# Kernel optimization log

Measured on AMD Instinct MI355X. Metric: run time of the kernel, lower is better.

The kernel has to match this reference:

```python
import jax, jax.numpy as jnp
import numpy as np

B_SZ, L, D_MODEL = 2, 2048, 2048
INTER, HEADS, P, N, G, K = 4096, 64, 64, 128, 1, 4
CONV_DIM = INTER + 2 * G * N
EPS = 1e-5


def silu(x):
    return x * jax.nn.sigmoid(x)


def softplus_thresh(x, threshold=10.0):
    # matches source: where(x < thr, log(1+exp(x)), x)
    return jnp.where(x < threshold, jnp.log1p(jnp.exp(jnp.minimum(x, threshold))), x)


def setup_inputs() -> dict:
    key = jax.random.key(0)
    ks = jax.random.split(key, 8)
    s = 0.02
    return {
        "hidden_states": jax.random.normal(ks[0], (B_SZ, L, D_MODEL), jnp.float32),
        "W_z": jax.random.normal(ks[1], (D_MODEL, INTER), jnp.float32) * s,
        "W_xBC": jax.random.normal(ks[2], (D_MODEL, CONV_DIM), jnp.float32) * s,
        "W_dt": jax.random.normal(ks[3], (D_MODEL, HEADS), jnp.float32) * s,
        "conv_w": jax.random.normal(ks[4], (CONV_DIM, K), jnp.float32) * 0.1,
        "conv_b": jnp.zeros((CONV_DIM,), jnp.float32),
        "dt_bias": jax.random.uniform(ks[5], (HEADS,), jnp.float32, -2.0, 0.0),
        "A_log": jnp.log(jnp.arange(1, HEADS + 1, dtype=jnp.float32)),
        "D": jnp.ones((HEADS,), jnp.float32),
        "norm_w": jnp.ones((INTER,), jnp.float32),
        "W_out": jax.random.normal(ks[6], (INTER, D_MODEL), jnp.float32) * s,
    }


def reference(hidden_states, W_z, W_xBC, W_dt, conv_w, conv_b, dt_bias, A_log, D, norm_w, W_out):
    b, l, _ = hidden_states.shape
    Hg = HEADS // G  # heads per group

    gate = hidden_states @ W_z                      # [b,l,INTER]
    xBC = hidden_states @ W_xBC                     # [b,l,CONV_DIM]
    dt = softplus_thresh(hidden_states @ W_dt + dt_bias)  # [b,l,H]

    # causal depthwise conv1d + silu (padding=K-1, truncated to seq_len)
    xp = jnp.pad(xBC, ((0, 0), (K - 1, 0), (0, 0)))
    kern = jnp.transpose(conv_w)[:, None, :]        # [K,1,CONV_DIM] (WIO)
    xBC = jax.lax.conv_general_dilated(
        xp, kern, (1,), 'VALID',
        dimension_numbers=('NWC', 'WIO', 'NWC'),
        feature_group_count=CONV_DIM)
    xBC = silu(xBC + conv_b)

    gns = G * N
    x = xBC[..., :INTER].reshape(b, l, G, Hg, P)
    Bm = xBC[..., INTER:INTER + gns].reshape(b, l, G, N)
    Cm = xBC[..., INTER + gns:].reshape(b, l, G, N)

    A = -jnp.exp(A_log)                             # [H]
    dA = jnp.exp(dt * A).reshape(b, l, G, Hg)       # [b,l,G,Hg]
    dtx = dt.reshape(b, l, G, Hg)[..., None] * x    # [b,l,G,Hg,P]

    def step(state, inp):
        dA_t, dtx_t, B_t, C_t = inp
        # state: [b,G,Hg,P,N]
        state = state * dA_t[..., None, None] + dtx_t[..., None] * B_t[:, :, None, None, :]
        y_t = jnp.einsum('bghpn,bgn->bghp', state, C_t)
        return state, y_t

    xs = (jnp.moveaxis(dA, 1, 0), jnp.moveaxis(dtx, 1, 0),
          jnp.moveaxis(Bm, 1, 0), jnp.moveaxis(Cm, 1, 0))
    state0 = jnp.zeros((b, G, Hg, P, N), jnp.float32)
    _, ys = jax.lax.scan(step, state0, xs)          # [l,b,G,Hg,P]
    y = jnp.moveaxis(ys, 0, 1) + D.reshape(G, Hg)[..., None] * x
    scan_out = y.reshape(b, l, INTER)

    # gated RMSNorm within groups
    hs = scan_out.reshape(b, l, G, INTER // G).astype(jnp.float32)
    gt = gate.reshape(b, l, G, INTER // G).astype(jnp.float32)
    hs = hs * silu(gt)
    var = jnp.mean(hs * hs, axis=-1, keepdims=True)
    hs = hs * jax.lax.rsqrt(var + EPS)
    normed = norm_w * hs.reshape(b, l, INTER)

    return normed @ W_out
```

## Files before the change

kernel.cpp:

```cpp
#include <hip/hip_runtime.h>
#include <hip/hip_bf16.h>
#include <math.h>

typedef unsigned short u16;
typedef unsigned int   u32;
typedef __attribute__((ext_vector_type(8))) short short8;
typedef __attribute__((ext_vector_type(4))) float f32x4;

#define B_SZ     2
#define LSEQ     2048
#define DMODEL   2048
#define INTER    4096
#define HEADS    64
#define NSTATE   128
#define CONV_DIM 4352
#define XSTR     8576
#define NFUSE    8576
#define EPS      1e-5f
#define QCH      64
#define NCHUNK   (LSEQ / QCH)

__device__ __forceinline__ float bf2f(u16 u) {
    u32 v = ((u32)u) << 16;
    return __builtin_bit_cast(float, v);
}
__device__ __forceinline__ u16 f2bf(float x) {
    __hip_bfloat16 h = __float2bfloat16(x);
    return __builtin_bit_cast(u16, h);
}
__device__ __forceinline__ u32 pack2(float lo, float hi) {
    return (u32)f2bf(lo) | ((u32)f2bf(hi) << 16);
}
__device__ __forceinline__ void gl2lds16(const void* g, void* l) {
    __builtin_amdgcn_global_load_lds(
        (const __attribute__((address_space(1))) u32*)g,
        (__attribute__((address_space(3))) u32*)l, 16, 0, 0);
}

__global__ __launch_bounds__(256) void cvt_f32_bf16(
    const float* __restrict__ in, u16* __restrict__ out, int n4)
{
    int i = blockIdx.x * 256 + threadIdx.x;
    if (i >= n4) return;
    float4 v = ((const float4*)in)[i];
    ushort4 o;
    o.x = f2bf(v.x); o.y = f2bf(v.y); o.z = f2bf(v.z); o.w = f2bf(v.w);
    ((ushort4*)out)[i] = o;
}

__global__ __launch_bounds__(256) void tr_f32_bf16(
    const float* __restrict__ in, u16* __restrict__ out, int R, int C)
{
    __shared__ u16 tile[64][68];
    const int r0 = blockIdx.y * 64, c0 = blockIdx.x * 64;
    const int tr = threadIdx.x >> 4, tc = (threadIdx.x & 15) * 4;
    #pragma unroll
    for (int i = 0; i < 4; ++i) {
        int r = tr + i * 16;
        float4 v = *(const float4*)(in + (size_t)(r0 + r) * C + c0 + tc);
        tile[r][tc + 0] = f2bf(v.x);
        tile[r][tc + 1] = f2bf(v.y);
        tile[r][tc + 2] = f2bf(v.z);
        tile[r][tc + 3] = f2bf(v.w);
    }
    __syncthreads();
    #pragma unroll
    for (int i = 0; i < 4; ++i) {
        int oc = tr + i * 16;
        ushort4 o;
        o.x = tile[tc + 0][oc];
        o.y = tile[tc + 1][oc];
        o.z = tile[tc + 2][oc];
        o.w = tile[tc + 3][oc];
        *(ushort4*)(out + (size_t)(c0 + oc) * R + r0 + tc) = o;
    }
}

template<int OUT_BF16>
__global__ __launch_bounds__(256) void gemm_nt(
    const u16* __restrict__ A, const u16* __restrict__ Bt,
    void* __restrict__ Co, int M, int N, int K, int lda)
{
    __shared__ __align__(16) u16 As[128 * 64];
    __shared__ __align__(16) u16 Bs[128 * 64];
    const int tid  = threadIdx.x;
    const int wave = tid >> 6, lane = tid & 63;
    const int m0 = blockIdx.y * 128, n0 = blockIdx.x * 128;
    const int wm = (wave >> 1) * 64, wn = (wave & 1) * 64;

    const int l3  = lane >> 3, lcb = lane & 7;
    const int swrow = wave * 32;
    const int scb8  = (lcb ^ l3) << 3;

    f32x4 acc[4][4];
    #pragma unroll
    for (int i = 0; i < 4; ++i)
        #pragma unroll
        for (int j = 0; j < 4; ++j) acc[i][j] = (f32x4)0.f;

    const int lr = lane & 15, lq = lane >> 4;

    for (int k0 = 0; k0 < K; k0 += 64) {
        __syncthreads();
        #pragma unroll
        for (int q = 0; q < 4; ++q) {
            int row = swrow + q * 8 + l3;
            gl2lds16(A  + (size_t)(m0 + row) * lda + scb8 + k0, As + (swrow + q * 8) * 64);
            gl2lds16(Bt + (size_t)(n0 + row) * K   + scb8 + k0, Bs + (swrow + q * 8) * 64);
        }
        __syncthreads();

        #pragma unroll
        for (int kk = 0; kk < 2; ++kk) {
            short8 af[4], bfr[4];
            #pragma unroll
            for (int i = 0; i < 4; ++i) {
                int row = wm + i * 16 + lr;
                int slot = (kk * 4 + lq) ^ (lr & 7);
                af[i] = *(const short8*)(As + row * 64 + slot * 8);
            }
            #pragma unroll
            for (int j = 0; j < 4; ++j) {
                int row = wn + j * 16 + lr;
                int slot = (kk * 4 + lq) ^ (lr & 7);
                bfr[j] = *(const short8*)(Bs + row * 64 + slot * 8);
            }
            #pragma unroll
            for (int i = 0; i < 4; ++i)
                #pragma unroll
                for (int j = 0; j < 4; ++j)
                    acc[i][j] = __builtin_amdgcn_mfma_f32_16x16x32_bf16(
                        af[i], bfr[j], acc[i][j], 0, 0, 0);
        }
    }

    const int odd  = lr & 1;
    #pragma unroll
    for (int i = 0; i < 4; ++i)
        #pragma unroll
        for (int j = 0; j < 4; ++j) {
            float v0 = acc[i][j][0], v1 = acc[i][j][1];
            float v2 = acc[i][j][2], v3 = acc[i][j][3];
            float n0v = __shfl_xor(v0, 1), n1v = __shfl_xor(v1, 1);
            float n2v = __shfl_xor(v2, 1), n3v = __shfl_xor(v3, 1);
            int colb  = n0 + wn + j * 16 + (lr & ~1);
            int rbase = m0 + wm + i * 16 + lq * 4 + odd * 2;
            if (OUT_BF16) {
                u32 w0 = odd ? pack2(n2v, v2) : pack2(v0, n0v);
                u32 w1 = odd ? pack2(n3v, v3) : pack2(v1, n1v);
                *(u32*)((u16*)Co + (size_t)rbase * N + colb) = w0;
                *(u32*)((u16*)Co + (size_t)(rbase + 1) * N + colb) = w1;
            } else {
                float2 f0 = odd ? make_float2(n2v, v2) : make_float2(v0, n0v);
                float2 f1 = odd ? make_float2(n3v, v3) : make_float2(v1, n1v);
                *(float2*)((float*)Co + (size_t)rbase * N + colb) = f0;
                *(float2*)((float*)Co + (size_t)(rbase + 1) * N + colb) = f1;
            }
        }
}

__global__ void dt_kernel(const u16* __restrict__ xall,
                          float* __restrict__ dtb,
                          const float* __restrict__ dt_bias, int n)
{
    int i = blockIdx.x * 256 + threadIdx.x;
    if (i >= n) return;
    int h = i & 63, row = i >> 6;
    float x = bf2f(xall[(size_t)row * XSTR + INTER + CONV_DIM + h]) + dt_bias[h];
    dtb[i] = (x < 10.f) ? log1pf(expf(x)) : x;
}

__global__ void conv_kernel(const u16* __restrict__ xall,
                            const float* __restrict__ cw,
                            const float* __restrict__ cb,
                            u16* __restrict__ xout)
{
    int c  = blockIdx.x * 256 + threadIdx.x;
    int bt = blockIdx.y;
    int t  = bt & (LSEQ - 1);
    const u16* xi = xall + (size_t)bt * XSTR + INTER + c;
    float4 w = *(const float4*)(cw + (size_t)c * 4);
    float acc = cb[c];
    acc = fmaf(bf2f(xi[0]), w.w, acc);
    if (t >= 1) acc = fmaf(bf2f(*(xi - XSTR)),     w.z, acc);
    if (t >= 2) acc = fmaf(bf2f(*(xi - 2 * XSTR)), w.y, acc);
    if (t >= 3) acc = fmaf(bf2f(*(xi - 3 * XSTR)), w.x, acc);
    xout[(size_t)bt * CONV_DIM + c] = f2bf(acc / (1.f + expf(-acc)));
}

__global__ __launch_bounds__(256) void ssd_chunk_state(
    const u16* __restrict__ xc, const float* __restrict__ dtb,
    const float* __restrict__ A_log,
    u16* __restrict__ Tg, float* __restrict__ decayQ)
{
    const int bid = blockIdx.x;
    const int b = bid >> 11, h = (bid >> 5) & 63, c = bid & 31;
    const int t0 = c * QCH;
    const int tid = threadIdx.x;
    const int wave = tid >> 6, lane = tid & 63;
    const int lr = lane & 15, lq = lane >> 4;

    __shared__ __align__(16) u16 BT[128][72];
    __shared__ __align__(16) u16 XwT[64][72];
    __shared__ float sclL[QCH];

    const u16* xg = xc + (size_t)b * LSEQ * CONV_DIM;

    if (tid < 64) {
        float dtv = dtb[((size_t)b * LSEQ + t0 + tid) * HEADS + h];
        float a = -dtv * expf(A_log[h]);
        float s = a;
        #pragma unroll
        for (int off = 1; off < 64; off <<= 1) {
            float o = __shfl_up(s, off, 64);
            if (tid >= off) s += o;
        }
        float cq = __shfl(s, 63, 64);
        sclL[tid] = dtv * expf(cq - s);
        if (tid == 0) decayQ[((b * 64 + h) << 5) + c] = expf(cq);
    }
    __syncthreads();

    #pragma unroll
    for (int r = 0; r < 16; ++r) {
        int idx = tid + 256 * r, j = idx >> 6, p = idx & 63;
        float v = bf2f(xg[(size_t)(t0 + j) * CONV_DIM + h * 64 + p]);
        XwT[p][j] = f2bf(v * sclL[j]);
    }
    #pragma unroll
    for (int r = 0; r < 32; ++r) {
        int idx = tid + 256 * r, j = idx >> 7, n = idx & 127;
        BT[n][j] = xg[(size_t)(t0 + j) * CONV_DIM + INTER + n];
    }
    __syncthreads();

    f32x4 acc[8];
    #pragma unroll
    for (int i = 0; i < 8; ++i) acc[i] = (f32x4)0.f;
    #pragma unroll
    for (int k0 = 0; k0 < QCH; k0 += 32) {
        short8 af = *(const short8*)&XwT[wave * 16 + lr][k0 + lq * 8];
        #pragma unroll
        for (int nt = 0; nt < 8; ++nt) {
            short8 bfr = *(const short8*)&BT[nt * 16 + lr][k0 + lq * 8];
            acc[nt] = __builtin_amdgcn_mfma_f32_16x16x32_bf16(af, bfr, acc[nt], 0, 0, 0);
        }
    }
    u16* To = Tg + ((((size_t)(b * 64 + h)) * NCHUNK + c) * 64) * 128;
    #pragma unroll
    for (int nt = 0; nt < 8; ++nt)
        #pragma unroll
        for (int r = 0; r < 4; ++r)
            To[(wave * 16 + lq * 4 + r) * 128 + nt * 16 + lr] = f2bf(acc[nt][r]);
}

__global__ __launch_bounds__(256) void ssd_state_scan(
    u16* __restrict__ Tg, const float* __restrict__ decayQ)
{
    const int bh = blockIdx.x, tid = threadIdx.x;
    const int p = tid >> 2, nb = (tid & 3) * 32;
    float S[32];
    #pragma unroll
    for (int m = 0; m < 32; ++m) S[m] = 0.f;

    for (int c = 0; c < NCHUNK; ++c) {
        u16* base = Tg + ((((size_t)bh * NCHUNK + c) * 64 + p) * 128) + nb;
        uint4 tv[4];
        #pragma unroll
        for (int k = 0; k < 4; ++k) tv[k] = *(const uint4*)(base + k * 8);
        #pragma unroll
        for (int k = 0; k < 4; ++k) {
            uint4 sv;
            sv.x = pack2(S[k*8+0], S[k*8+1]);
            sv.y = pack2(S[k*8+2], S[k*8+3]);
            sv.z = pack2(S[k*8+4], S[k*8+5]);
            sv.w = pack2(S[k*8+6], S[k*8+7]);
            *(uint4*)(base + k * 8) = sv;
        }
        float dq = decayQ[(bh << 5) + c];
        #pragma unroll
        for (int k = 0; k < 4; ++k) {
            const u32* w = (const u32*)&tv[k];
            #pragma unroll
            for (int e = 0; e < 4; ++e) {
                S[k*8 + e*2]     = fmaf(dq, S[k*8 + e*2],     bf2f((u16)(w[e] & 0xffffu)));
                S[k*8 + e*2 + 1] = fmaf(dq, S[k*8 + e*2 + 1], bf2f((u16)(w[e] >> 16)));
            }
        }
    }
}

__global__ __launch_bounds__(256) void ssd_output(
    const u16* __restrict__ xc, const float* __restrict__ dtb,
    const float* __restrict__ A_log, const float* __restrict__ Dvec,
    const u16* __restrict__ Sg,
    u16* __restrict__ y)
{
    const int bid = blockIdx.x;
    const int b = bid >> 11, h = (bid >> 5) & 63, c = bid & 31;
    const int t0 = c * QCH;
    const int tid = threadIdx.x;
    const int wave = tid >> 6, lane = tid & 63;
    const int lr = lane & 15, lq = lane >> 4;

    __shared__ __align__(16) u16 C_lds[64][136];
    __shared__ __align__(16) u16 B_lds[64][136];
    __shared__ __align__(16) u16 S_lds[64][136];
    __shared__ __align__(16) u16 P_lds[64][72];
    __shared__ __align__(16) u16 XT[64][72];
    __shared__ float cumL[QCH], dtsL[QCH], escL[QCH];

    const u16* xg = xc + (size_t)b * LSEQ * CONV_DIM;

    if (tid < 64) {
        float dtv = dtb[((size_t)b * LSEQ + t0 + tid) * HEADS + h];
        float a = -dtv * expf(A_log[h]);
        float s = a;
        #pragma unroll
        for (int off = 1; off < 64; off <<= 1) {
            float o = __shfl_up(s, off, 64);
            if (tid >= off) s += o;
        }
        cumL[tid] = s;
        dtsL[tid] = dtv;
        escL[tid] = expf(s);
    }
    #pragma unroll
    for (int r4 = 0; r4 < 4; ++r4) {
        int idx4 = tid + 256 * r4;
        int j = idx4 >> 4, c8 = (idx4 & 15) * 8;
        *(uint4*)&B_lds[j][c8] = *(const uint4*)(xg + (size_t)(t0 + j) * CONV_DIM + INTER + c8);
        *(uint4*)&C_lds[j][c8] = *(const uint4*)(xg + (size_t)(t0 + j) * CONV_DIM + INTER + NSTATE + c8);
        *(uint4*)&S_lds[j][c8] = *(const uint4*)(Sg + ((((size_t)(b * 64 + h)) * NCHUNK + c) * 64 + j) * 128 + c8);
    }
    #pragma unroll
    for (int r = 0; r < 16; ++r) {
        int idx = tid + 256 * r, j = idx >> 6, p = idx & 63;
        XT[p][j] = xg[(size_t)(t0 + j) * CONV_DIM + h * 64 + p];
    }
    __syncthreads();

    f32x4 accG[4];
    #pragma unroll
    for (int i = 0; i < 4; ++i) accG[i] = (f32x4)0.f;
    #pragma unroll
    for (int k0 = 0; k0 < NSTATE; k0 += 32) {
        short8 af = *(const short8*)&C_lds[wave * 16 + lr][k0 + lq * 8];
        #pragma unroll
        for (int jt = 0; jt < 4; ++jt) {
            short8 bfr = *(const short8*)&B_lds[jt * 16 + lr][k0 + lq * 8];
            accG[jt] = __builtin_amdgcn_mfma_f32_16x16x32_bf16(af, bfr, accG[jt], 0, 0, 0);
        }
    }
    #pragma unroll
    for (int jt = 0; jt < 4; ++jt)
        #pragma unroll
        for (int r = 0; r < 4; ++r) {
            int ii = wave * 16 + lq * 4 + r;
            int jj = jt * 16 + lr;
            float v = (jj <= ii)
                ? accG[jt][r] * dtsL[jj] * expf(cumL[ii] - cumL[jj]) : 0.f;
            P_lds[ii][jj] = f2bf(v);
        }
    __syncthreads();

    f32x4 accY[4], accZ[4];
    #pragma unroll
    for (int i = 0; i < 4; ++i) { accY[i] = (f32x4)0.f; accZ[i] = (f32x4)0.f; }
    #pragma unroll
    for (int k0 = 0; k0 < QCH; k0 += 32) {
        short8 af = *(const short8*)&P_lds[wave * 16 + lr][k0 + lq * 8];
        #pragma unroll
        for (int pt = 0; pt < 4; ++pt) {
            short8 bfr = *(const short8*)&XT[pt * 16 + lr][k0 + lq * 8];
            accY[pt] = __builtin_amdgcn_mfma_f32_16x16x32_bf16(af, bfr, accY[pt], 0, 0, 0);
        }
    }
    #pragma unroll
    for (int k0 = 0; k0 < NSTATE; k0 += 32) {
        short8 af = *(const short8*)&C_lds[wave * 16 + lr][k0 + lq * 8];
        #pragma unroll
        for (int pt = 0; pt < 4; ++pt) {
            short8 bfr = *(const short8*)&S_lds[pt * 16 + lr][k0 + lq * 8];
            accZ[pt] = __builtin_amdgcn_mfma_f32_16x16x32_bf16(af, bfr, accZ[pt], 0, 0, 0);
        }
    }

    const float Dh = Dvec[h];
    u16* yg = y + ((size_t)b * LSEQ + t0) * XSTR + h * 64;
    #pragma unroll
    for (int pt = 0; pt < 4; ++pt)
        #pragma unroll
        for (int r = 0; r < 4; ++r) {
            int ii = wave * 16 + lq * 4 + r;
            int pp = pt * 16 + lr;
            float xv = bf2f(XT[pp][ii]);
            float o = accY[pt][r] + escL[ii] * accZ[pt][r] + Dh * xv;
            yg[(size_t)ii * XSTR + pp] = f2bf(o);
        }
}

__global__ __launch_bounds__(256) void norm_kernel(
    u16* __restrict__ xall, const float* __restrict__ w)
{
    const int row = blockIdx.x;
    const u16* yr = xall + (size_t)row * XSTR + INTER;
    u16*       gr = xall + (size_t)row * XSTR;
    const int tid = threadIdx.x;

    float v[16];
    float ss = 0.f;
    #pragma unroll
    for (int i = 0; i < 16; ++i) {
        int idx = tid + i * 256;
        float hv = bf2f(yr[idx]);
        float g  = bf2f(gr[idx]);
        float val = hv * (g / (1.f + expf(-g)));
        v[i] = val;
        ss = fmaf(val, val, ss);
    }
    #pragma unroll
    for (int o = 32; o > 0; o >>= 1) ss += __shfl_xor(ss, o);
    __shared__ float part[4];
    if ((tid & 63) == 0) part[tid >> 6] = ss;
    __syncthreads();
    float tot  = part[0] + part[1] + part[2] + part[3];
    float rinv = rsqrtf(tot * (1.f / INTER) + EPS);
    #pragma unroll
    for (int i = 0; i < 16; ++i) {
        int idx = tid + i * 256;
        gr[idx] = f2bf(w[idx] * v[i] * rinv);
    }
}

extern "C" void kernel_launch(void* const* d_in, const int* in_sizes, int n_in,
                              void* d_out, int out_size, void* d_ws, size_t ws_size,
                              hipStream_t stream)
{
    const float* hs      = (const float*)d_in[0];
    const float* W_z     = (const float*)d_in[1];
    const float* W_xBC   = (const float*)d_in[2];
    const float* W_dt    = (const float*)d_in[3];
    const float* conv_w  = (const float*)d_in[4];
    const float* conv_b  = (const float*)d_in[5];
    const float* dt_bias = (const float*)d_in[6];
    const float* A_log   = (const float*)d_in[7];
    const float* Dv      = (const float*)d_in[8];
    const float* norm_w  = (const float*)d_in[9];
    const float* W_out   = (const float*)d_in[10];
    float* out = (float*)d_out;
    char*  w8  = (char*)d_ws;

    u16* hs_bf  = (u16*)(w8 + 0);
    u16* Wt_all = (u16*)(w8 + 16777216);
    u16* Tbuf   = (u16*)(w8 + 0);
    u16* Wt_out = (u16*)(w8 + 67108864);
    u16* xall   = (u16*)(w8 + 83886080);
    u16* xconv  = (u16*)(w8 + 154140672);
    float* dtb  = (float*)(w8 + 189792256);
    float* dcq  = (float*)(w8 + 190840832);

    const int M = B_SZ * LSEQ;

    cvt_f32_bf16<<<(M * DMODEL / 4 + 255) / 256, 256, 0, stream>>>(hs, hs_bf, M * DMODEL / 4);
    tr_f32_bf16<<<dim3(INTER / 64,    DMODEL / 64), 256, 0, stream>>>(W_z,   Wt_all, DMODEL, INTER);
    tr_f32_bf16<<<dim3(CONV_DIM / 64, DMODEL / 64), 256, 0, stream>>>(W_xBC, Wt_all + (size_t)INTER * DMODEL, DMODEL, CONV_DIM);
    tr_f32_bf16<<<dim3(1,             DMODEL / 64), 256, 0, stream>>>(W_dt,  Wt_all + (size_t)(INTER + CONV_DIM) * DMODEL, DMODEL, 64);
    hipMemsetAsync(Wt_all + (size_t)(INTER + CONV_DIM + 64) * DMODEL, 0, (size_t)64 * DMODEL * 2, stream);
    tr_f32_bf16<<<dim3(DMODEL / 64,   INTER / 64),  256, 0, stream>>>(W_out, Wt_out, INTER, DMODEL);

    gemm_nt<1><<<dim3(NFUSE / 128, M / 128), 256, 0, stream>>>(
        hs_bf, Wt_all, (void*)xall, M, NFUSE, DMODEL, DMODEL);

    dt_kernel<<<(M * HEADS + 255) / 256, 256, 0, stream>>>(xall, dtb, dt_bias, M * HEADS);
    conv_kernel<<<dim3(CONV_DIM / 256, M), 256, 0, stream>>>(xall, conv_w, conv_b, xconv);

    ssd_chunk_state<<<B_SZ * HEADS * NCHUNK, 256, 0, stream>>>(xconv, dtb, A_log, Tbuf, dcq);
    ssd_state_scan<<<B_SZ * HEADS, 256, 0, stream>>>(Tbuf, dcq);
    ssd_output<<<B_SZ * HEADS * NCHUNK, 256, 0, stream>>>(xconv, dtb, A_log, Dv, Tbuf, xall + INTER);

    norm_kernel<<<M, 256, 0, stream>>>(xall, norm_w);

    gemm_nt<0><<<dim3(DMODEL / 128, M / 128), 256, 0, stream>>>(
        xall, Wt_out, (void*)out, M, DMODEL, INTER, XSTR);
}
```

Before: 652.4 us.

## Replace GEMMs with 256x256 double-buffered pipelined kernel and split-K output projection

Both GEMMs move to a new 512-thread kernel with 256x256 tiles, a two-stage LDS buffer and phased prefetch interleaved with MFMA under manual s_waitcnt/barrier scheduling. It also adds an XCD-aware block swizzle. The fused input projection's N is padded to 8704 with extra zeroed weight rows, and stores past the real width are masked. The output projection is split-K in two, writing fp32 partials to workspace that an extra add kernel sums, trading extra memory traffic for more parallelism.

```diff
diff --git a/kernel.cpp b/kernel.cpp
--- a/kernel.cpp
+++ b/kernel.cpp
@@ -15,7 +15,7 @@
 #define NSTATE   128
 #define CONV_DIM 4352
 #define XSTR     8576
-#define NFUSE    8576
+#define NFUSE    8704
 #define EPS      1e-5f
 #define QCH      64
 #define NCHUNK   (LSEQ / QCH)
@@ -76,87 +76,144 @@
     }
 }
 
+#define SA(c) (smem + (c) * 32768)
+#define SB(c) (smem + (c) * 32768 + 16384)
+#define STGA(c, q, ko) gl2lds16(gA + (size_t)((q) * 64) * lda + (ko), SA(c) + (q) * 4096 + lbase)
+#define STGB(c, q, ko) gl2lds16(gB + (size_t)((q) * 64) * ldb + (ko), SB(c) + (q) * 4096 + lbase)
+
+#define PH(mh, kk, READB, STAGES, TAIL)                                          \
+  {                                                                              \
+    short8 af[4];                                                                \
+    _Pragma("unroll")                                                            \
+    for (int i_ = 0; i_ < 4; ++i_)                                               \
+      af[i_] = *(const short8*)(Ab + (wm * 128 + (mh) * 64 + i_ * 16 + lr) * 64  \
+                                + ((((kk) * 4 + lq) ^ (lr & 7)) << 3));          \
+    if (READB) {                                                                 \
+      _Pragma("unroll")                                                          \
+      for (int j_ = 0; j_ < 4; ++j_)                                             \
+        bfr[kk][j_] = *(const short8*)(Bb + (wn * 64 + j_ * 16 + lr) * 64        \
+                                       + ((((kk) * 4 + lq) ^ (lr & 7)) << 3));   \
+    }                                                                            \
+    STAGES                                                                       \
+    __builtin_amdgcn_sched_barrier(0);                                           \
+    __builtin_amdgcn_s_barrier();                                                \
+    asm volatile("s_waitcnt lgkmcnt(0)" ::: "memory");                           \
+    __builtin_amdgcn_sched_barrier(0);                                           \
+    __builtin_amdgcn_s_setprio(1);                                               \
+    _Pragma("unroll")                                                            \
+    for (int i_ = 0; i_ < 4; ++i_)                                               \
+      _Pragma("unroll")                                                          \
+      for (int j_ = 0; j_ < 4; ++j_)                                             \
+        acc[(mh) * 4 + i_][j_] = __builtin_amdgcn_mfma_f32_16x16x32_bf16(        \
+            af[i_], bfr[kk][j_], acc[(mh) * 4 + i_][j_], 0, 0, 0);               \
+    __builtin_amdgcn_s_setprio(0);                                               \
+    __builtin_amdgcn_sched_barrier(0);                                           \
+    TAIL                                                                         \
+    __builtin_amdgcn_s_barrier();                                                \
+  }
+
+#define TILE(tt, c)                                                              \
+  {                                                                              \
+    const int t_ = (tt);                                                         \
+    const int k1_ = (t_ + 1) << 6, k2_ = (t_ + 2) << 6;                          \
+    const bool st1_ = (t_ + 1 < nt), st2_ = (t_ + 2 < nt);                       \
+    const u16* Ab = SA(c); const u16* Bb = SB(c);                                \
+    PH(0, 0, 1, { if (st1_) { STGA((c) ^ 1, 1, k1_); STGA((c) ^ 1, 3, k1_); } }, {}) \
+    PH(1, 0, 0, { if (st1_) { STGB((c) ^ 1, 0, k1_); STGB((c) ^ 1, 1, k1_); } }, {}) \
+    PH(0, 1, 1, { if (st1_) { STGB((c) ^ 1, 2, k1_); STGB((c) ^ 1, 3, k1_); } }, {}) \
+    PH(1, 1, 0, { if (st2_) { STGA((c), 0, k2_); STGA((c), 2, k2_); } },         \
+       { if (t_ < nt - 1) {                                                      \
+           if (st2_) { asm volatile("s_waitcnt vmcnt(2)" ::: "memory"); }        \
+           else      { asm volatile("s_waitcnt vmcnt(0)" ::: "memory"); } } })   \
+  }
+
 template<int OUT_BF16>
-__global__ __launch_bounds__(256) void gemm_nt(
-    const u16* __restrict__ A, const u16* __restrict__ Bt,
-    void* __restrict__ Co, int M, int N, int K, int lda)
-{
-    __shared__ __align__(16) u16 As[128 * 64];
-    __shared__ __align__(16) u16 Bs[128 * 64];
+__global__ __launch_bounds__(512, 2) void gemm8(
+    const u16* __restrict__ A, const u16* __restrict__ Bt, void* __restrict__ Co,
+    int K, int lda, int ldb, int ldc, int Nstore)
+{
+    __shared__ __align__(16) u16 smem[65536];
     const int tid  = threadIdx.x;
     const int wave = tid >> 6, lane = tid & 63;
-    const int m0 = blockIdx.y * 128, n0 = blockIdx.x * 128;
-    const int wm = (wave >> 1) * 64, wn = (wave & 1) * 64;
-
-    const int l3  = lane >> 3, lcb = lane & 7;
-    const int swrow = wave * 32;
-    const int scb8  = (lcb ^ l3) << 3;
-
-    f32x4 acc[4][4];
-    #pragma unroll
-    for (int i = 0; i < 4; ++i)
+    const int wm = wave >> 2, wn = wave & 3;
+    const int lr = lane & 15, lq = lane >> 4;
+
+    const int nbx = gridDim.x;
+    const int bid = blockIdx.y * nbx + blockIdx.x;
+    const int nwg = nbx * gridDim.y;
+    const int cpx = nwg >> 3;
+    const int swz = (bid & 7) * cpx + (bid >> 3);
+    const int n0 = (swz % nbx) * 256;
+    const int m0 = (swz / nbx) * 256;
+    const int kbase = blockIdx.z * K;
+
+    const int srow  = tid >> 3;
+    const int scb8  = ((tid & 7) ^ (srow & 7)) << 3;
+    const int lbase = (tid >> 6) << 9;
+    const u16* gA = A  + (size_t)(m0 + srow) * lda + kbase + scb8;
+    const u16* gB = Bt + (size_t)(n0 + srow) * ldb + kbase + scb8;
+
+    f32x4 acc[8][4];
+    #pragma unroll
+    for (int i = 0; i < 8; ++i)
         #pragma unroll
         for (int j = 0; j < 4; ++j) acc[i][j] = (f32x4)0.f;
-
-    const int lr = lane & 15, lq = lane >> 4;
-
-    for (int k0 = 0; k0 < K; k0 += 64) {
-        __syncthreads();
-        #pragma unroll
-        for (int q = 0; q < 4; ++q) {
-            int row = swrow + q * 8 + l3;
-            gl2lds16(A  + (size_t)(m0 + row) * lda + scb8 + k0, As + (swrow + q * 8) * 64);
-            gl2lds16(Bt + (size_t)(n0 + row) * K   + scb8 + k0, Bs + (swrow + q * 8) * 64);
-        }
-        __syncthreads();
-
-        #pragma unroll
-        for (int kk = 0; kk < 2; ++kk) {
-            short8 af[4], bfr[4];
-            #pragma unroll
-            for (int i = 0; i < 4; ++i) {
-                int row = wm + i * 16 + lr;
-                int slot = (kk * 4 + lq) ^ (lr & 7);
-                af[i] = *(const short8*)(As + row * 64 + slot * 8);
-            }
-            #pragma unroll
-            for (int j = 0; j < 4; ++j) {
-                int row = wn + j * 16 + lr;
-                int slot = (kk * 4 + lq) ^ (lr & 7);
-                bfr[j] = *(const short8*)(Bs + row * 64 + slot * 8);
-            }
-            #pragma unroll
-            for (int i = 0; i < 4; ++i)
-                #pragma unroll
-                for (int j = 0; j < 4; ++j)
-                    acc[i][j] = __builtin_amdgcn_mfma_f32_16x16x32_bf16(
-                        af[i], bfr[j], acc[i][j], 0, 0, 0);
-        }
-    }
-
-    const int odd  = lr & 1;
-    #pragma unroll
-    for (int i = 0; i < 4; ++i)
+    short8 bfr[2][4];
+
+    const int nt = K >> 6;
+
+    STGA(0, 0, 0); STGA(0, 1, 0); STGA(0, 2, 0); STGA(0, 3, 0);
+    STGB(0, 0, 0); STGB(0, 1, 0); STGB(0, 2, 0); STGB(0, 3, 0);
+    STGA(1, 0, 64); STGA(1, 2, 64);
+    __builtin_amdgcn_sched_barrier(0);
+    asm volatile("s_waitcnt vmcnt(2)" ::: "memory");
+    __builtin_amdgcn_sched_barrier(0);
+    __builtin_amdgcn_s_barrier();
+
+    for (int t = 0; t < nt; t += 2) {
+        TILE(t, 0)
+        TILE(t + 1, 1)
+    }
+
+    const int odd = lr & 1;
+    const bool wstore = (n0 + wn * 64) < Nstore;
+    #pragma unroll
+    for (int i = 0; i < 8; ++i)
         #pragma unroll
         for (int j = 0; j < 4; ++j) {
             float v0 = acc[i][j][0], v1 = acc[i][j][1];
             float v2 = acc[i][j][2], v3 = acc[i][j][3];
             float n0v = __shfl_xor(v0, 1), n1v = __shfl_xor(v1, 1);
             float n2v = __shfl_xor(v2, 1), n3v = __shfl_xor(v3, 1);
-            int colb  = n0 + wn + j * 16 + (lr & ~1);
-            int rbase = m0 + wm + i * 16 + lq * 4 + odd * 2;
-            if (OUT_BF16) {
-                u32 w0 = odd ? pack2(n2v, v2) : pack2(v0, n0v);
-                u32 w1 = odd ? pack2(n3v, v3) : pack2(v1, n1v);
-                *(u32*)((u16*)Co + (size_t)rbase * N + colb) = w0;
-                *(u32*)((u16*)Co + (size_t)(rbase + 1) * N + colb) = w1;
-            } else {
-                float2 f0 = odd ? make_float2(n2v, v2) : make_float2(v0, n0v);
-                float2 f1 = odd ? make_float2(n3v, v3) : make_float2(v1, n1v);
-                *(float2*)((float*)Co + (size_t)rbase * N + colb) = f0;
-                *(float2*)((float*)Co + (size_t)(rbase + 1) * N + colb) = f1;
+            int colb  = n0 + wn * 64 + j * 16 + (lr & ~1);
+            int rbase = m0 + wm * 128 + i * 16 + lq * 4 + odd * 2;
+            if (wstore) {
+                if (OUT_BF16) {
+                    u32 w0 = odd ? pack2(n2v, v2) : pack2(v0, n0v);
+                    u32 w1 = odd ? pack2(n3v, v3) : pack2(v1, n1v);
+                    *(u32*)((u16*)Co + (size_t)rbase * ldc + colb) = w0;
+                    *(u32*)((u16*)Co + (size_t)(rbase + 1) * ldc + colb) = w1;
+                } else {
+                    float* Cf = (float*)Co + (size_t)blockIdx.z * 4096 * ldc;
+                    float2 f0 = odd ? make_float2(n2v, v2) : make_float2(v0, n0v);
+                    float2 f1 = odd ? make_float2(n3v, v3) : make_float2(v1, n1v);
+                    *(float2*)(Cf + (size_t)rbase * ldc + colb) = f0;
+                    *(float2*)(Cf + (size_t)(rbase + 1) * ldc + colb) = f1;
+                }
             }
         }
+}
+
+__global__ __launch_bounds__(256) void add2_f32(
+    const float* __restrict__ a, const float* __restrict__ b,
+    float* __restrict__ o, int n4)
+{
+    int i = blockIdx.x * 256 + threadIdx.x;
+    if (i >= n4) return;
+    float4 x = ((const float4*)a)[i];
+    float4 y = ((const float4*)b)[i];
+    x.x += y.x; x.y += y.y; x.z += y.z; x.w += y.w;
+    ((float4*)o)[i] = x;
 }
 
 __global__ void dt_kernel(const u16* __restrict__ xall,
@@ -454,6 +511,7 @@
     u16* hs_bf  = (u16*)(w8 + 0);
     u16* Wt_all = (u16*)(w8 + 16777216);
     u16* Tbuf   = (u16*)(w8 + 0);
+    float* Cpart= (float*)(w8 + 0);
     u16* Wt_out = (u16*)(w8 + 67108864);
     u16* xall   = (u16*)(w8 + 83886080);
     u16* xconv  = (u16*)(w8 + 154140672);
@@ -466,11 +524,12 @@
     tr_f32_bf16<<<dim3(INTER / 64,    DMODEL / 64), 256, 0, stream>>>(W_z,   Wt_all, DMODEL, INTER);
     tr_f32_bf16<<<dim3(CONV_DIM / 64, DMODEL / 64), 256, 0, stream>>>(W_xBC, Wt_all + (size_t)INTER * DMODEL, DMODEL, CONV_DIM);
     tr_f32_bf16<<<dim3(1,             DMODEL / 64), 256, 0, stream>>>(W_dt,  Wt_all + (size_t)(INTER + CONV_DIM) * DMODEL, DMODEL, 64);
-    hipMemsetAsync(Wt_all + (size_t)(INTER + CONV_DIM + 64) * DMODEL, 0, (size_t)64 * DMODEL * 2, stream);
+    hipMemsetAsync(Wt_all + (size_t)(INTER + CONV_DIM + 64) * DMODEL, 0, (size_t)192 * DMODEL * 2, stream);
     tr_f32_bf16<<<dim3(DMODEL / 64,   INTER / 64),  256, 0, stream>>>(W_out, Wt_out, INTER, DMODEL);
 
-    gemm_nt<1><<<dim3(NFUSE / 128, M / 128), 256, 0, stream>>>(
-        hs_bf, Wt_all, (void*)xall, M, NFUSE, DMODEL, DMODEL);
+    gemm8<1><<<dim3(NFUSE / 256, M / 256, 1), 512, 0, stream>>>(
+        hs_bf, Wt_all, (void*)xall, DMODEL , DMODEL , DMODEL ,
+        XSTR , XSTR );
 
     dt_kernel<<<(M * HEADS + 255) / 256, 256, 0, stream>>>(xall, dtb, dt_bias, M * HEADS);
     conv_kernel<<<dim3(CONV_DIM / 256, M), 256, 0, stream>>>(xall, conv_w, conv_b, xconv);
@@ -481,6 +540,9 @@
 
     norm_kernel<<<M, 256, 0, stream>>>(xall, norm_w);
 
-    gemm_nt<0><<<dim3(DMODEL / 128, M / 128), 256, 0, stream>>>(
-        xall, Wt_out, (void*)out, M, DMODEL, INTER, XSTR);
-}
+    gemm8<0><<<dim3(DMODEL / 256, M / 256, 2), 512, 0, stream>>>(
+        xall, Wt_out, (void*)Cpart, INTER / 2 , XSTR ,
+        INTER , DMODEL , DMODEL );
+    add2_f32<<<(M * DMODEL / 4 + 255) / 256, 256, 0, stream>>>(
+        Cpart, Cpart + (size_t)M * DMODEL, out, M * DMODEL / 4);
+}
```

Result: faster. 638.6 us (-2.1%).
